# Performance work log

Measured on AMD Instinct MI355X. Metric: run time of the kernel, lower is better.

## Reference

```python
import jax, jax.numpy as jnp
import numpy as np

N = 50000
E = 800000
IN_C = 512
HID = 256
NUM_CLASS = (10, 25, 16, 350)


def _glorot(key, shape):
    fan_in, fan_out = shape[0], shape[1]
    lim = float(np.sqrt(6.0 / (fan_in + fan_out)))
    return jax.random.uniform(key, shape, jnp.float32, -lim, lim)


def setup_inputs() -> dict:
    key = jax.random.key(0)
    ks = jax.random.split(key, 16)
    x = jax.random.normal(ks[0], (N, IN_C), jnp.float32)
    edge_index = jax.random.randint(ks[1], (2, E), 0, N, jnp.int32)
    inp = {"x": x, "edge_index": edge_index}
    # gc1
    inp["W1"] = _glorot(ks[2], (IN_C, HID)); inp["b1"] = jnp.zeros((HID,), jnp.float32)
    # four GCNConv heads
    names = ["type", "school", "time", "author"]
    for i, (nm, nc) in enumerate(zip(names, NUM_CLASS)):
        inp[f"Wg_{nm}"] = _glorot(ks[3 + i], (HID, nc))
        inp[f"bg_{nm}"] = jnp.zeros((nc,), jnp.float32)
        inp[f"Wc_{nm}"] = _glorot(ks[7 + i], (nc, nc))
        inp[f"bc_{nm}"] = jnp.zeros((nc,), jnp.float32)
    return inp


def gcn_conv(x, W, b, src, dst, n):
    # GCNConv: out = D^{-1/2} (A + I) D^{-1/2} (x W) + b, symmetric norm.
    xw = x @ W  # [N, out]
    ones = jnp.ones((src.shape[0],), xw.dtype)
    deg = jax.ops.segment_sum(ones, dst, num_segments=n) + 1.0  # +1 from self-loop
    dinv = jax.lax.rsqrt(deg)
    norm = dinv[src] * dinv[dst]  # [E]
    agg = jax.ops.segment_sum(xw[src] * norm[:, None], dst, num_segments=n)
    # self-loop contribution: norm_ii = dinv_i^2
    return agg + xw * (dinv * dinv)[:, None] + b


def reference(x, edge_index, W1, b1,
              Wg_type, bg_type, Wc_type, bc_type,
              Wg_school, bg_school, Wc_school, bc_school,
              Wg_time, bg_time, Wc_time, bc_time,
              Wg_author, bg_author, Wc_author, bc_author):
    src, dst = edge_index[0], edge_index[1]
    n = x.shape[0]
    h = jax.nn.relu(gcn_conv(x, W1, b1, src, dst, n))  # dropout is identity in eval

    def head(Wg, bg, Wc, bc):
        g = gcn_conv(h, Wg, bg, src, dst, n)
        return jax.nn.softmax(g @ Wc + bc, axis=-1)

    out_type = head(Wg_type, bg_type, Wc_type, bc_type)
    out_school = head(Wg_school, bg_school, Wc_school, bc_school)
    out_time = head(Wg_time, bg_time, Wc_time, bc_time)
    out_author = head(Wg_author, bg_author, Wc_author, bc_author)
    return (out_type, out_school, out_time, out_author)
```

## Files before the change

kernel.cpp:

```cpp
#include <hip/hip_runtime.h>
#include <hip/hip_bf16.h>
#include <cstdint>
#include <cstddef>
#include <math.h>

#define NN 50000
#define NE 800000
#define INC 512
#define HIDC 256
#define NBLK ((NN + 255) / 256)

typedef __attribute__((ext_vector_type(8))) short s8v;
typedef __attribute__((ext_vector_type(4))) float f4v;

__device__ __forceinline__ float b2f(unsigned short u) {
    return __uint_as_float(((unsigned)u) << 16);
}
__device__ __forceinline__ unsigned short f2b(float f) {
    __hip_bfloat16 h = __float2bfloat16(f);
    return *reinterpret_cast<unsigned short*>(&h);
}

__global__ void k_deg_count(const int* __restrict__ dst, int* __restrict__ cnt, int e) {
    int i = blockIdx.x * 256 + threadIdx.x;
    if (i < e) atomicAdd(&cnt[dst[i]], 1);
}
__global__ void k_scan1(const int* __restrict__ cnt, int* __restrict__ excl,
                        int* __restrict__ bsum, float* __restrict__ dinv, int n) {
    __shared__ int s[256];
    int i = blockIdx.x * 256 + threadIdx.x;
    int v = (i < n) ? cnt[i] : 0;
    if (i < n) dinv[i] = rsqrtf((float)v + 1.0f);
    s[threadIdx.x] = v;
    __syncthreads();
    for (int off = 1; off < 256; off <<= 1) {
        int t = (threadIdx.x >= off) ? s[threadIdx.x - off] : 0;
        __syncthreads();
        s[threadIdx.x] += t;
        __syncthreads();
    }
    if (i < n) excl[i] = s[threadIdx.x] - v;
    if (threadIdx.x == 255) bsum[blockIdx.x] = s[255];
}
__global__ void k_scan2(int* __restrict__ bsum, int* __restrict__ bsumx, int nb) {
    __shared__ int s[256];
    int t = threadIdx.x;
    int v = (t < nb) ? bsum[t] : 0;
    s[t] = v;
    __syncthreads();
    for (int off = 1; off < 256; off <<= 1) {
        int tt = (t >= off) ? s[t - off] : 0;
        __syncthreads();
        s[t] += tt;
        __syncthreads();
    }
    if (t < nb) bsumx[t] = s[t] - v;
}
__global__ void k_scan3(int* __restrict__ rowptr, const int* __restrict__ bsumx, int n, int e) {
    int i = blockIdx.x * 256 + threadIdx.x;
    if (i < n) rowptr[i] += bsumx[blockIdx.x];
    if (i == 0) rowptr[n] = e;
}
__global__ void k_fill(const int* __restrict__ src, const int* __restrict__ dst,
                       const int* __restrict__ rowptr, int* __restrict__ cursor,
                       int* __restrict__ col, int e) {
    int i = blockIdx.x * 256 + threadIdx.x;
    if (i >= e) return;
    int d = dst[i];
    int pos = rowptr[d] + atomicAdd(&cursor[d], 1);
    col[pos] = src[i];
}

__global__ void k_tr2(const float* __restrict__ Wg3, const float* __restrict__ Wc3,
                      float* __restrict__ Wg3t, float* __restrict__ Wc3t) {
    int t = blockIdx.x * 256 + threadIdx.x;
    if (t < 256 * 350) { int k = t / 350, i = t - k * 350; Wg3t[i * 256 + k] = Wg3[t]; }
    if (t < 350 * 350) { int i = t / 350, j = t - i * 350; Wc3t[j * 350 + i] = Wc3[t]; }
}

__global__ void k_prep(const float* __restrict__ W1,
                       const float* __restrict__ Wg0, const float* __restrict__ Wc0,
                       const float* __restrict__ bg0, const float* __restrict__ bc0,
                       const float* __restrict__ Wg1, const float* __restrict__ Wc1,
                       const float* __restrict__ bg1, const float* __restrict__ bc1,
                       const float* __restrict__ Wg2, const float* __restrict__ Wc2,
                       const float* __restrict__ bg2, const float* __restrict__ bc2,
                       const float* __restrict__ Wg3, const float* __restrict__ Wc3,
                       const float* __restrict__ bg3, const float* __restrict__ bc3,
                       const float* __restrict__ Wg3t, const float* __restrict__ Wc3t,
                       unsigned short* __restrict__ W1t, unsigned short* __restrict__ Wft,
                       float* __restrict__ bfv)
{
    __shared__ float Wcj[352];
    int b = blockIdx.x, tid = threadIdx.x;
    if (b < 512) {
        int t = b * 256 + tid;
        int c = t >> 9, k = t & 511;
        W1t[(size_t)c * 512 + k] = f2b(W1[(size_t)k * 256 + c]);
    } else if (b < 960) {
        int j = b - 512, k = tid;
        float s = 0.f;
        if (j < 350) {
            for (int i = tid; i < 350; i += 256) Wcj[i] = Wc3t[(size_t)j * 350 + i];
            __syncthreads();
            for (int i = 0; i < 350; ++i) s += Wg3t[i * 256 + k] * Wcj[i];
        } else if (j >= 352 && j < 362) {
            int jj = j - 352; for (int i = 0; i < 10; ++i) s += Wg0[k * 10 + i] * Wc0[i * 10 + jj];
        } else if (j >= 362 && j < 387) {
            int jj = j - 362; for (int i = 0; i < 25; ++i) s += Wg1[k * 25 + i] * Wc1[i * 25 + jj];
        } else if (j >= 387 && j < 403) {
            int jj = j - 387; for (int i = 0; i < 16; ++i) s += Wg2[k * 16 + i] * Wc2[i * 16 + jj];
        }
        Wft[(size_t)j * 256 + k] = f2b(s);
    } else {
        int j = (b - 960) * 256 + tid;
        if (j >= 448) return;
        float s = 0.f;
        if (j < 350)                  { s = bc3[j]; for (int i = 0; i < 350; ++i) s += bg3[i] * Wc3[(size_t)i * 350 + j]; }
        else if (j >= 352 && j < 362) { int jj = j - 352; s = bc0[jj]; for (int i = 0; i < 10; ++i) s += bg0[i] * Wc0[i * 10 + jj]; }
        else if (j >= 362 && j < 387) { int jj = j - 362; s = bc1[jj]; for (int i = 0; i < 25; ++i) s += bg1[i] * Wc1[i * 25 + jj]; }
        else if (j >= 387 && j < 403) { int jj = j - 387; s = bc2[jj]; for (int i = 0; i < 16; ++i) s += bg2[i] * Wc2[i * 16 + jj]; }
        bfv[j] = s;
    }
}

__global__ __launch_bounds__(512) void gemm1_conv(
    const float* __restrict__ X, const unsigned short* __restrict__ Bt,
    unsigned short* __restrict__ C, int M)
{
    __shared__ s8v As[1024];
    __shared__ s8v Bs[2048];
    const int t = threadIdx.x;
    const int lane = t & 63, wv = t >> 6;
    const int row0 = blockIdx.x * 128;
    const int l15 = lane & 15, lq = lane >> 4, l7 = lane & 7;

    f4v acc[16] = {};
    for (int k0 = 0; k0 < 512; k0 += 64) {
#pragma unroll
        for (int s = 0; s < 2; ++s) {
            int c = s * 512 + t;
            int row = c >> 3, ch = c & 7;
            int chg = ch ^ (row & 7);
            int gr = row0 + row; if (gr >= M) gr = M - 1;
            const float* src = X + (size_t)gr * 512 + k0 + chg * 8;
            float4 a = *(const float4*)src;
            float4 b = *(const float4*)(src + 4);
            s8v o;
            o[0] = (short)f2b(a.x); o[1] = (short)f2b(a.y);
            o[2] = (short)f2b(a.z); o[3] = (short)f2b(a.w);
            o[4] = (short)f2b(b.x); o[5] = (short)f2b(b.y);
            o[6] = (short)f2b(b.z); o[7] = (short)f2b(b.w);
            As[c] = o;
        }
#pragma unroll
        for (int s = 0; s < 4; ++s) {
            int c = s * 512 + t;
            int colr = c >> 3, ch = c & 7;
            int chg = ch ^ (colr & 7);
            Bs[c] = *(const s8v*)(Bt + (size_t)colr * 512 + k0 + chg * 8);
        }
        __syncthreads();
#pragma unroll
        for (int kk = 0; kk < 2; ++kk) {
            s8v af = As[(wv * 16 + l15) * 8 + ((kk * 4 + lq) ^ l7)];
#pragma unroll
            for (int cf = 0; cf < 16; ++cf) {
                s8v bfr = Bs[(cf * 16 + l15) * 8 + ((kk * 4 + lq) ^ l7)];
                acc[cf] = __builtin_amdgcn_mfma_f32_16x16x32_bf16(af, bfr, acc[cf], 0, 0, 0);
            }
        }
        __syncthreads();
    }
#pragma unroll
    for (int cf = 0; cf < 16; ++cf)
#pragma unroll
        for (int r = 0; r < 4; ++r) {
            int row = row0 + wv * 16 + lq * 4 + r;
            if (row < M) C[(size_t)row * 256 + cf * 16 + l15] = f2b(acc[cf][r]);
        }
}

template <bool RELU, bool BIAS>
__global__ __launch_bounds__(256) void k_gather2(
    const unsigned short* __restrict__ feat, const int* __restrict__ rowptr,
    const int* __restrict__ col, const float* __restrict__ dinv,
    const float* __restrict__ bias, unsigned short* __restrict__ out, int n)
{
    int unit = (blockIdx.x * 256 + threadIdx.x) >> 5;
    int l32 = threadIdx.x & 31;
    if (unit >= n) return;
    float di = dinv[unit];
    int p0 = rowptr[unit], p1 = rowptr[unit + 1];
    int deg = p1 - p0;
    int myc = 0; float mydj = 0.f;
    if (l32 < deg) { myc = col[p0 + l32]; mydj = dinv[myc]; }
    float acc[8] = {};
    int dmin = deg < 32 ? deg : 32;
    int base = threadIdx.x & 32;
#pragma unroll 2
    for (int q = 0; q < dmin; ++q) {
        int j = __shfl(myc, base + q);
        float dj = __shfl(mydj, base + q);
        s8v v = *(const s8v*)(feat + (size_t)j * HIDC + l32 * 8);
#pragma unroll
        for (int c = 0; c < 8; ++c) acc[c] += dj * b2f((unsigned short)v[c]);
    }
    for (int p = p0 + 32; p < p1; ++p) {
        int j = col[p];
        float dj = dinv[j];
        s8v v = *(const s8v*)(feat + (size_t)j * HIDC + l32 * 8);
#pragma unroll
        for (int c = 0; c < 8; ++c) acc[c] += dj * b2f((unsigned short)v[c]);
    }
    s8v sv = *(const s8v*)(feat + (size_t)unit * HIDC + l32 * 8);
    float dd = di * di;
    s8v o;
#pragma unroll
    for (int c = 0; c < 8; ++c) {
        float r = di * acc[c] + dd * b2f((unsigned short)sv[c]);
        if (BIAS) r += bias[l32 * 8 + c];
        if (RELU) r = fmaxf(r, 0.f);
        o[c] = (short)f2b(r);
    }
    *(s8v*)(out + (size_t)unit * HIDC + l32 * 8) = o;
}

__global__ __launch_bounds__(512) void gemm2_heads(
    const unsigned short* __restrict__ A, const unsigned short* __restrict__ Bt,
    const float* __restrict__ bfv,
    float* __restrict__ o0, float* __restrict__ o1,
    float* __restrict__ o2, float* __restrict__ o3, int M)
{
    __shared__ s8v As[1024];
    __shared__ s8v Bs[3584];
    const int t = threadIdx.x;
    const int lane = t & 63, wv = t >> 6;
    const int row0 = blockIdx.x * 128;
    const int l15 = lane & 15, lq = lane >> 4, l7 = lane & 7;

    f4v acc[28] = {};
    for (int k0 = 0; k0 < 256; k0 += 64) {
#pragma unroll
        for (int s = 0; s < 2; ++s) {
            int c = s * 512 + t;
            int row = c >> 3, ch = c & 7;
            int chg = ch ^ (row & 7);
            int gr = row0 + row; if (gr >= M) gr = M - 1;
            As[c] = *(const s8v*)(A + (size_t)gr * 256 + k0 + chg * 8);
        }
#pragma unroll
        for (int s = 0; s < 7; ++s) {
            int c = s * 512 + t;
            int colr = c >> 3, ch = c & 7;
            int chg = ch ^ (colr & 7);
            Bs[c] = *(const s8v*)(Bt + (size_t)colr * 256 + k0 + chg * 8);
        }
        __syncthreads();
#pragma unroll
        for (int kk = 0; kk < 2; ++kk) {
            s8v af = As[(wv * 16 + l15) * 8 + ((kk * 4 + lq) ^ l7)];
#pragma unroll
            for (int cf = 0; cf < 28; ++cf) {
                s8v bfr = Bs[(cf * 16 + l15) * 8 + ((kk * 4 + lq) ^ l7)];
                acc[cf] = __builtin_amdgcn_mfma_f32_16x16x32_bf16(af, bfr, acc[cf], 0, 0, 0);
            }
        }
        __syncthreads();
    }
#pragma unroll
    for (int cf = 0; cf < 28; ++cf) {
        float b = bfv[cf * 16 + l15];
#pragma unroll
        for (int r = 0; r < 4; ++r) acc[cf][r] += b;
    }
#pragma unroll
    for (int r = 0; r < 4; ++r) {
        int row = row0 + wv * 16 + lq * 4 + r;
        float m0 = -1e30f, m1 = -1e30f, m2 = -1e30f, m3 = -1e30f;
#pragma unroll
        for (int cf = 0; cf < 28; ++cf) {
            int colc = cf * 16 + l15;
            float xv = acc[cf][r];
            if (colc < 350) m0 = fmaxf(m0, xv);
            else if (colc >= 352 && colc < 362) m1 = fmaxf(m1, xv);
            else if (colc >= 362 && colc < 387) m2 = fmaxf(m2, xv);
            else if (colc >= 387 && colc < 403) m3 = fmaxf(m3, xv);
        }
#pragma unroll
        for (int o = 8; o; o >>= 1) {
            m0 = fmaxf(m0, __shfl_xor(m0, o));
            m1 = fmaxf(m1, __shfl_xor(m1, o));
            m2 = fmaxf(m2, __shfl_xor(m2, o));
            m3 = fmaxf(m3, __shfl_xor(m3, o));
        }
        float s0 = 0.f, s1 = 0.f, s2 = 0.f, s3 = 0.f;
#pragma unroll
        for (int cf = 0; cf < 28; ++cf) {
            int colc = cf * 16 + l15;
            float xv = acc[cf][r];
            float e = 0.f;
            if (colc < 350)                     { e = __expf(xv - m0); s0 += e; }
            else if (colc >= 352 && colc < 362) { e = __expf(xv - m1); s1 += e; }
            else if (colc >= 362 && colc < 387) { e = __expf(xv - m2); s2 += e; }
            else if (colc >= 387 && colc < 403) { e = __expf(xv - m3); s3 += e; }
            acc[cf][r] = e;
        }
#pragma unroll
        for (int o = 8; o; o >>= 1) {
            s0 += __shfl_xor(s0, o); s1 += __shfl_xor(s1, o);
            s2 += __shfl_xor(s2, o); s3 += __shfl_xor(s3, o);
        }
        float i0 = 1.f / s0, i1 = 1.f / s1, i2 = 1.f / s2, i3 = 1.f / s3;
        if (row < M) {
#pragma unroll
            for (int cf = 0; cf < 28; ++cf) {
                int colc = cf * 16 + l15;
                float e = acc[cf][r];
                if (colc < 350)                     o3[(size_t)row * 350 + colc]       = e * i0;
                else if (colc >= 352 && colc < 362) o0[(size_t)row * 10 + colc - 352]  = e * i1;
                else if (colc >= 362 && colc < 387) o1[(size_t)row * 25 + colc - 362]  = e * i2;
                else if (colc >= 387 && colc < 403) o2[(size_t)row * 16 + colc - 387]  = e * i3;
            }
        }
    }
}

extern "C" void kernel_launch(void* const* d_in, const int* in_sizes, int n_in,
                              void* d_out, int out_size, void* d_ws, size_t ws_size,
                              hipStream_t stream)
{
    const float* x   = (const float*)d_in[0];
    const int*   ei  = (const int*)d_in[1];
    const float* W1  = (const float*)d_in[2];
    const float* b1  = (const float*)d_in[3];
    const float* Wg0 = (const float*)d_in[4];
    const float* bg0 = (const float*)d_in[5];
    const float* Wc0 = (const float*)d_in[6];
    const float* bc0 = (const float*)d_in[7];
    const float* Wg1 = (const float*)d_in[8];
    const float* bg1 = (const float*)d_in[9];
    const float* Wc1 = (const float*)d_in[10];
    const float* bc1 = (const float*)d_in[11];
    const float* Wg2 = (const float*)d_in[12];
    const float* bg2 = (const float*)d_in[13];
    const float* Wc2 = (const float*)d_in[14];
    const float* bc2 = (const float*)d_in[15];
    const float* Wg3 = (const float*)d_in[16];
    const float* bg3 = (const float*)d_in[17];
    const float* Wc3 = (const float*)d_in[18];
    const float* bc3 = (const float*)d_in[19];
    const int* srcI = ei;
    const int* dstI = ei + NE;

    char* ws = (char*)d_ws;
    size_t off = 0;
    auto alloc = [&](size_t bytes) { void* p = ws + off; off += (bytes + 255) & ~(size_t)255; return p; };
    float* dinv   = (float*)alloc(50176 * 4);
    int*   rowptr = (int*)  alloc(50432 * 4);
    int*   cnt    = (int*)  alloc(2 * 50176 * 4);
    int*   cursor = cnt + 50176;
    int*   bsum   = (int*)  alloc(1024);
    int*   bsumx  = (int*)  alloc(1024);
    int*   col    = (int*)  alloc((size_t)NE * 4);
    unsigned short* W1t = (unsigned short*)alloc(256 * 512 * 2);
    unsigned short* Wft = (unsigned short*)alloc(448 * 256 * 2);
    float* bfv   = (float*)alloc(448 * 4);
    float* Wg3t  = (float*)alloc(350 * 256 * 4);
    float* Wc3t  = (float*)alloc(350 * 350 * 4);
    unsigned short* xwb = (unsigned short*)alloc((size_t)NN * HIDC * 2);
    unsigned short* hb  = (unsigned short*)alloc((size_t)NN * HIDC * 2);
    unsigned short* ahb = xwb;

    float* out0 = (float*)d_out;
    float* out1 = out0 + (size_t)NN * 10;
    float* out2 = out1 + (size_t)NN * 25;
    float* out3 = out2 + (size_t)NN * 16;

    hipMemsetAsync(cnt, 0, 2 * 50176 * 4, stream);
    k_deg_count<<<(NE + 255) / 256, 256, 0, stream>>>(dstI, cnt, NE);
    k_scan1<<<NBLK, 256, 0, stream>>>(cnt, rowptr, bsum, dinv, NN);
    k_scan2<<<1, 256, 0, stream>>>(bsum, bsumx, NBLK);
    k_scan3<<<NBLK, 256, 0, stream>>>(rowptr, bsumx, NN, NE);
    k_fill<<<(NE + 255) / 256, 256, 0, stream>>>(srcI, dstI, rowptr, cursor, col, NE);

    k_tr2<<<(350 * 350 + 255) / 256, 256, 0, stream>>>(Wg3, Wc3, Wg3t, Wc3t);
    k_prep<<<962, 256, 0, stream>>>(W1,
                                    Wg0, Wc0, bg0, bc0, Wg1, Wc1, bg1, bc1,
                                    Wg2, Wc2, bg2, bc2, Wg3, Wc3, bg3, bc3,
                                    Wg3t, Wc3t, W1t, Wft, bfv);

    gemm1_conv<<<(NN + 127) / 128, 512, 0, stream>>>(x, W1t, xwb, NN);
    k_gather2<true, true><<<(NN + 7) / 8, 256, 0, stream>>>(xwb, rowptr, col, dinv, b1, hb, NN);
    k_gather2<false, false><<<(NN + 7) / 8, 256, 0, stream>>>(hb, rowptr, col, dinv, nullptr, ahb, NN);
    gemm2_heads<<<(NN + 127) / 128, 512, 0, stream>>>(ahb, Wft, bfv, out0, out1, out2, out3, NN);
}
```

Measured before the change: 321.2 us.

## Fuse second neighbor aggregation into head GEMM kernel via shared-memory A tile

Replaces the separate second gather pass and the heads GEMM with one kernel. Each 64-row block first aggregates neighbor features from the CSR graph directly into a swizzled shared-memory A tile, then runs the MFMA GEMM against the fused head weights. This avoids writing and re-reading the aggregated N×256 bf16 intermediate and saves a kernel launch. In exchange, tiles are smaller (64 rows, 256 threads), the B tile is reloaded per k-slice, and gather latency is not overlapped with MFMA work.

```diff
diff --git a/kernel.cpp b/kernel.cpp
--- a/kernel.cpp
+++ b/kernel.cpp
@@ -226,48 +226,75 @@
     *(s8v*)(out + (size_t)unit * HIDC + l32 * 8) = o;
 }
 
-__global__ __launch_bounds__(512) void gemm2_heads(
-    const unsigned short* __restrict__ A, const unsigned short* __restrict__ Bt,
-    const float* __restrict__ bfv,
+__global__ __launch_bounds__(256) void k_gg2(
+    const unsigned short* __restrict__ feat, const int* __restrict__ rowptr,
+    const int* __restrict__ col, const float* __restrict__ dinv,
+    const unsigned short* __restrict__ Bt, const float* __restrict__ bfv,
     float* __restrict__ o0, float* __restrict__ o1,
     float* __restrict__ o2, float* __restrict__ o3, int M)
 {
-    __shared__ s8v As[1024];
-    __shared__ s8v Bs[3584];
+    __shared__ s8v As[2048];
+    __shared__ s8v Bs[1792];
     const int t = threadIdx.x;
     const int lane = t & 63, wv = t >> 6;
-    const int row0 = blockIdx.x * 128;
+    const int l32 = lane & 31, half = lane >> 5, base = lane & 32;
+    const int row0 = blockIdx.x * 64;
     const int l15 = lane & 15, lq = lane >> 4, l7 = lane & 7;
 
+    for (int it = 0; it < 8; ++it) {
+        int lrow = wv * 16 + it * 2 + half;
+        int nd = row0 + lrow; if (nd >= M) nd = M - 1;
+        float di = dinv[nd];
+        int p0 = rowptr[nd], p1 = rowptr[nd + 1];
+        int deg = p1 - p0;
+        int myc = 0; float mydj = 0.f;
+        if (l32 < deg) { myc = col[p0 + l32]; mydj = dinv[myc]; }
+        float acc[8] = {};
+        int dmin = deg < 32 ? deg : 32;
+#pragma unroll 4
+        for (int q = 0; q < dmin; ++q) {
+            int j = __shfl(myc, base + q);
+            float dj = __shfl(mydj, base + q);
+            s8v v = *(const s8v*)(feat + (size_t)j * HIDC + l32 * 8);
+#pragma unroll
+            for (int c = 0; c < 8; ++c) acc[c] += dj * b2f((unsigned short)v[c]);
+        }
+        for (int p = p0 + 32; p < p1; ++p) {
+            int j = col[p];
+            float dj = dinv[j];
+            s8v v = *(const s8v*)(feat + (size_t)j * HIDC + l32 * 8);
+#pragma unroll
+            for (int c = 0; c < 8; ++c) acc[c] += dj * b2f((unsigned short)v[c]);
+        }
+        s8v sv = *(const s8v*)(feat + (size_t)nd * HIDC + l32 * 8);
+        float dd = di * di;
+        s8v o;
+#pragma unroll
+        for (int c = 0; c < 8; ++c)
+            o[c] = (short)f2b(di * acc[c] + dd * b2f((unsigned short)sv[c]));
+        As[lrow * 32 + (l32 & 24) + ((l32 & 7) ^ (lrow & 7))] = o;
+    }
+    __syncthreads();
+
     f4v acc[28] = {};
-    for (int k0 = 0; k0 < 256; k0 += 64) {
-#pragma unroll
-        for (int s = 0; s < 2; ++s) {
-            int c = s * 512 + t;
-            int row = c >> 3, ch = c & 7;
-            int chg = ch ^ (row & 7);
-            int gr = row0 + row; if (gr >= M) gr = M - 1;
-            As[c] = *(const s8v*)(A + (size_t)gr * 256 + k0 + chg * 8);
-        }
+    for (int kg = 0; kg < 8; ++kg) {
 #pragma unroll
         for (int s = 0; s < 7; ++s) {
-            int c = s * 512 + t;
-            int colr = c >> 3, ch = c & 7;
-            int chg = ch ^ (colr & 7);
-            Bs[c] = *(const s8v*)(Bt + (size_t)colr * 256 + k0 + chg * 8);
-        }
-        __syncthreads();
-#pragma unroll
-        for (int kk = 0; kk < 2; ++kk) {
-            s8v af = As[(wv * 16 + l15) * 8 + ((kk * 4 + lq) ^ l7)];
-#pragma unroll
-            for (int cf = 0; cf < 28; ++cf) {
-                s8v bfr = Bs[(cf * 16 + l15) * 8 + ((kk * 4 + lq) ^ l7)];
-                acc[cf] = __builtin_amdgcn_mfma_f32_16x16x32_bf16(af, bfr, acc[cf], 0, 0, 0);
-            }
-        }
-        __syncthreads();
-    }
+            int idx = s * 256 + t;
+            int pl = idx & 3, cj = idx >> 2;
+            Bs[pl * 448 + (cj ^ (pl * 2))] =
+                *(const s8v*)(Bt + (size_t)cj * 256 + kg * 32 + pl * 8);
+        }
+        __syncthreads();
+        s8v af = As[(wv * 16 + l15) * 32 + (kg >> 1) * 8 + (((kg & 1) * 4 + lq) ^ l7)];
+#pragma unroll
+        for (int cf = 0; cf < 28; ++cf) {
+            s8v bfr = Bs[lq * 448 + ((cf * 16 + l15) ^ (lq * 2))];
+            acc[cf] = __builtin_amdgcn_mfma_f32_16x16x32_bf16(af, bfr, acc[cf], 0, 0, 0);
+        }
+        __syncthreads();
+    }
+
 #pragma unroll
     for (int cf = 0; cf < 28; ++cf) {
         float b = bfv[cf * 16 + l15];
@@ -370,7 +397,6 @@
     float* Wc3t  = (float*)alloc(350 * 350 * 4);
     unsigned short* xwb = (unsigned short*)alloc((size_t)NN * HIDC * 2);
     unsigned short* hb  = (unsigned short*)alloc((size_t)NN * HIDC * 2);
-    unsigned short* ahb = xwb;
 
     float* out0 = (float*)d_out;
     float* out1 = out0 + (size_t)NN * 10;
@@ -392,6 +418,6 @@
 
     gemm1_conv<<<(NN + 127) / 128, 512, 0, stream>>>(x, W1t, xwb, NN);
     k_gather2<true, true><<<(NN + 7) / 8, 256, 0, stream>>>(xwb, rowptr, col, dinv, b1, hb, NN);
-    k_gather2<false, false><<<(NN + 7) / 8, 256, 0, stream>>>(hb, rowptr, col, dinv, nullptr, ahb, NN);
-    gemm2_heads<<<(NN + 127) / 128, 512, 0, stream>>>(ahb, Wft, bfv, out0, out1, out2, out3, NN);
-}
+    k_gg2<<<(NN + 63) / 64, 256, 0, stream>>>(hb, rowptr, col, dinv, Wft, bfv,
+                                              out0, out1, out2, out3, NN);
+}
```

Result: slower. 372.4 us (+15.9%).
